# Optimization experiments

Measured on AMD Instinct MI355X. Metric: run time of the kernel, lower is better.

Reference implementation:

```python
import jax, jax.numpy as jnp
import numpy as np

N0, N1, N2 = 100000, 20000, 4000   # src(block0), dst(block0)=src(block1), dst(block1)
R = 3                               # number of relations
E0, E1 = 160000, 64000              # edges per relation per block
IN_FEATS, HID = 128, 128
TSS, RS = 64, 64
NTOT = 200000                       # global node count for tss/rs embed tables
F_IN = HID + TSS + RS               # IGConv input feature dim = 256


def _lin(key, fi, fo):
    k1, k2 = jax.random.split(key)
    s = float(1.0 / np.sqrt(fi))
    w = jax.random.uniform(k1, (fi, fo), minval=-s, maxval=s, dtype=jnp.float32)
    b = jax.random.uniform(k2, (fo,), minval=-s, maxval=s, dtype=jnp.float32)
    return w, b


def setup_inputs() -> dict:
    ks = jax.random.split(jax.random.key(0), 32)
    inp = {}
    inp["x_user"] = jax.random.normal(ks[0], (N0, IN_FEATS), dtype=jnp.float32)
    inp["tss_embed"] = jax.random.normal(ks[1], (NTOT, TSS), dtype=jnp.float32)
    inp["rs_embed"] = jax.random.normal(ks[2], (NTOT, RS), dtype=jnp.float32)
    inp["src_nid0"] = jax.random.randint(ks[3], (N0,), 0, NTOT)
    inp["src_nid1"] = jax.random.randint(ks[4], (N1,), 0, NTOT)
    inp["e0_src"] = jax.random.randint(ks[5], (R, E0), 0, N0)
    inp["e0_dst"] = jax.random.randint(ks[6], (R, E0), 0, N1)
    inp["e1_src"] = jax.random.randint(ks[7], (R, E1), 0, N1)
    inp["e1_dst"] = jax.random.randint(ks[8], (R, E1), 0, N2)
    inp["embed_w"], inp["embed_b"] = _lin(ks[9], IN_FEATS, HID)
    i = 10
    for l in (1, 2):
        for nm, fi in (("fc1", F_IN), ("fc2", 3 * F_IN), ("fc3", 2 * HID)):
            pw, pb = zip(*[_lin(jax.random.fold_in(ks[i], r), fi, HID) for r in range(R)])
            inp["l%d_%s_w" % (l, nm)] = jnp.stack(pw)  # [R, fi, HID]
            inp["l%d_%s_b" % (l, nm)] = jnp.stack(pb)  # [R, HID]
            i += 1
    inp["attn_w1"], inp["attn_b1"] = _lin(ks[i], HID, HID)
    inp["attn_w2"] = _lin(ks[i + 1], HID, 1)[0]  # Linear(hid,1,bias=False)
    inp["pred_w"], inp["pred_b"] = _lin(ks[i + 2], HID, 1)
    return inp


def _igconv(src_feat, dst_feat, esrc, edst, n_dst, fc1w, fc1b, fc2w, fc2b, fc3w, fc3b):
    # copy_u gather then max/mean/sum segment reductions over destination nodes
    m = src_feat[esrc]                                   # [E, F]
    s = jax.ops.segment_sum(m, edst, num_segments=n_dst)
    deg = jax.ops.segment_sum(jnp.ones(esrc.shape, m.dtype), edst, num_segments=n_dst)
    mean = s / jnp.maximum(deg, 1.0)[:, None]
    mx = jax.ops.segment_max(m, edst, num_segments=n_dst)
    mx = jnp.where(deg[:, None] > 0, mx, jnp.zeros_like(mx))  # DGL zeros for isolated dst
    msg = jnp.concatenate([mx, mean, s], axis=1)         # [n_dst, 3F]
    inp = jnp.concatenate([msg @ fc2w + fc2b, dst_feat @ fc1w + fc1b], axis=1)
    return jax.nn.relu(inp) @ fc3w + fc3b                # [n_dst, HID]


def _attn(z, w1, b1, w2):
    # SemanticAttention: z [N, R, HID]
    w = (jnp.tanh(z @ w1 + b1) @ w2).mean(0)             # [R, 1]
    beta = jax.nn.softmax(w, axis=0)                     # [R, 1]
    return (beta[None] * z).sum(1)                       # [N, HID]


def _forward(x_user, tss_embed, rs_embed, embed_w, embed_b,
             l1_fc1_w, l1_fc1_b, l1_fc2_w, l1_fc2_b, l1_fc3_w, l1_fc3_b,
             l2_fc1_w, l2_fc1_b, l2_fc2_w, l2_fc2_b, l2_fc3_w, l2_fc3_b,
             attn_w1, attn_b1, attn_w2, pred_w, pred_b,
             src_nid0, src_nid1, e0_src, e0_dst, e1_src, e1_dst):
    u0 = x_user @ embed_w + embed_b                      # self.embed
    feat0 = jnp.concatenate([u0, tss_embed[src_nid0], rs_embed[src_nid0]], axis=1)  # [N0,256]
    conv1 = jax.vmap(lambda es, ed, w1, b1, w2, b2, w3, b3:
                     _igconv(feat0, feat0[:N1], es, ed, N1, w1, b1, w2, b2, w3, b3))
    z1 = conv1(e0_src, e0_dst, l1_fc1_w, l1_fc1_b, l1_fc2_w, l1_fc2_b, l1_fc3_w, l1_fc3_b)  # [R,N1,HID]
    h1 = jax.nn.relu(_attn(jnp.transpose(z1, (1, 0, 2)), attn_w1, attn_b1, attn_w2))  # [N1,HID]
    feat1 = jnp.concatenate([h1, tss_embed[src_nid1], rs_embed[src_nid1]], axis=1)    # [N1,256]
    conv2 = jax.vmap(lambda es, ed, w1, b1, w2, b2, w3, b3:
                     _igconv(feat1, feat1[:N2], es, ed, N2, w1, b1, w2, b2, w3, b3))
    z2 = conv2(e1_src, e1_dst, l2_fc1_w, l2_fc1_b, l2_fc2_w, l2_fc2_b, l2_fc3_w, l2_fc3_b)  # [R,N2,HID]
    h2 = _attn(jnp.transpose(z2, (1, 0, 2)), attn_w1, attn_b1, attn_w2)              # [N2,HID]
    return jax.nn.sigmoid(h2 @ pred_w + pred_b)          # [N2,1]


def reference(x_user, tss_embed, rs_embed, src_nid0, src_nid1,
              e0_src, e0_dst, e1_src, e1_dst, embed_w, embed_b,
              l1_fc1_w, l1_fc1_b, l1_fc2_w, l1_fc2_b, l1_fc3_w, l1_fc3_b,
              l2_fc1_w, l2_fc1_b, l2_fc2_w, l2_fc2_b, l2_fc3_w, l2_fc3_b,
              attn_w1, attn_b1, attn_w2, pred_w, pred_b):
    return _forward(x_user, tss_embed, rs_embed, embed_w, embed_b,
                    l1_fc1_w, l1_fc1_b, l1_fc2_w, l1_fc2_b, l1_fc3_w, l1_fc3_b,
                    l2_fc1_w, l2_fc1_b, l2_fc2_w, l2_fc2_b, l2_fc3_w, l2_fc3_b,
                    attn_w1, attn_b1, attn_w2, pred_w, pred_b,
                    src_nid0, src_nid1, e0_src, e0_dst, e1_src, e1_dst)
```

## Files before the change

### kernel.cpp

```cpp
#include <hip/hip_runtime.h>
#include <math.h>


typedef short s16x8 __attribute__((ext_vector_type(8)));
typedef float f32x4 __attribute__((ext_vector_type(4)));

__device__ __forceinline__ ushort f2bf(float f) {
  unsigned u = __float_as_uint(f);
  return (ushort)((u + 0x7FFFu + ((u >> 16) & 1u)) >> 16);
}
__device__ __forceinline__ float bf2f(unsigned hbits) {
  return __uint_as_float(hbits << 16);
}
__device__ __forceinline__ unsigned pack2(float lo, float hi) {
  return (unsigned)f2bf(lo) | ((unsigned)f2bf(hi) << 16);
}

struct PrepAll {
  const float* src[8];
  ushort* dst[8];
  int K[8];
  int total[8];
};

__global__ __launch_bounds__(256) void prep_all(PrepAll P)
{
  int t = blockIdx.z;
  int off = blockIdx.x * 256 + threadIdx.x;
  if (off >= P.total[t]) return;
  int K = P.K[t];
  int k = off % K;
  int n = (off / K) & 127;
  int r = off / (K * 128);
  P.dst[t][off] = f2bf(P.src[t][((size_t)r * K + k) * 128 + n]);
}

struct GemmDesc {
  const void* A; int lda; size_t aStride; int aKind;
  const ushort* Wt; size_t wStride;
  const float* bias; int biasStride;
  void* C; int ldc; size_t cStride; int cKind;
  int M, K, relu;
  const ushort* aggM; const ushort* aggS; const float* invdeg;
  size_t aggStride; int invStride;
  const int* gnid; const float* gtss; const float* grs;
};

__global__ __launch_bounds__(256) void gemm_mfma(GemmDesc d0, GemmDesc d1)
{
  const GemmDesc d = blockIdx.z ? d1 : d0;
  const int r = blockIdx.y;
  __shared__ ushort As[128 * 32];
  __shared__ ushort Bs[128 * 32];

  const int tid = threadIdx.x;
  const int wave = tid >> 6, lane = tid & 63;
  const int m16 = lane & 15, quad = lane >> 4;
  const int rowBase = blockIdx.x * 128;
  const ushort* Wt = d.Wt + (size_t)r * d.wStride;

  f32x4 acc[2][8];
  #pragma unroll
  for (int i = 0; i < 2; ++i)
    #pragma unroll
    for (int j = 0; j < 8; ++j)
      #pragma unroll
      for (int p = 0; p < 4; ++p) acc[i][j][p] = 0.f;

  for (int k0 = 0; k0 < d.K; k0 += 32) {
    __syncthreads();
    if (d.aKind == 1) {
      const ushort* Ab = (const ushort*)d.A + (size_t)r * d.aStride;
      #pragma unroll
      for (int i = 0; i < 2; ++i) {
        int q = tid + 256 * i;
        int row = q >> 2, c = (q & 3) * 8;
        int grow = rowBase + row;
        uint4 v = make_uint4(0, 0, 0, 0);
        if (grow < d.M) v = *(const uint4*)(Ab + (size_t)grow * d.lda + k0 + c);
        *(uint4*)&As[row * 32 + c] = v;
      }
    } else if (d.aKind == 0) {
      const float* Ab = (const float*)d.A + (size_t)r * d.aStride;
      #pragma unroll
      for (int i = 0; i < 4; ++i) {
        int q = tid + 256 * i;
        int row = q >> 3, c = (q & 7) * 4;
        int grow = rowBase + row;
        float4 f = make_float4(0.f, 0.f, 0.f, 0.f);
        if (grow < d.M) f = *(const float4*)(Ab + (size_t)grow * d.lda + k0 + c);
        uint2 pk; pk.x = pack2(f.x, f.y); pk.y = pack2(f.z, f.w);
        *(uint2*)&As[row * 32 + c] = pk;
      }
    } else {
      int seg = k0 >> 8, jj = k0 & 255;
      const ushort* Ab = (seg == 0 ? d.aggM : d.aggS) + (size_t)r * d.aggStride;
      const float* idg = d.invdeg + (size_t)r * d.invStride;
      #pragma unroll
      for (int i = 0; i < 2; ++i) {
        int q = tid + 256 * i;
        int row = q >> 2, c = (q & 3) * 8;
        int grow = rowBase + row;
        uint4 v = make_uint4(0, 0, 0, 0);
        if (grow < d.M) {
          v = *(const uint4*)(Ab + (size_t)grow * 256 + jj + c);
          if (seg == 1) {
            float s = idg[grow];
            v.x = pack2(bf2f(v.x & 0xFFFFu) * s, bf2f(v.x >> 16) * s);
            v.y = pack2(bf2f(v.y & 0xFFFFu) * s, bf2f(v.y >> 16) * s);
            v.z = pack2(bf2f(v.z & 0xFFFFu) * s, bf2f(v.z >> 16) * s);
            v.w = pack2(bf2f(v.w & 0xFFFFu) * s, bf2f(v.w >> 16) * s);
          }
        }
        *(uint4*)&As[row * 32 + c] = v;
      }
    }
    #pragma unroll
    for (int i = 0; i < 2; ++i) {
      int q = tid + 256 * i;
      int col = q >> 2, c = (q & 3) * 8;
      uint4 v = *(const uint4*)(Wt + (size_t)col * d.K + k0 + c);
      *(uint4*)&Bs[col * 32 + c] = v;
    }
    __syncthreads();

    s16x8 af[2], bfr[8];
    af[0] = *(const s16x8*)&As[(wave * 32 + m16) * 32 + quad * 8];
    af[1] = *(const s16x8*)&As[(wave * 32 + 16 + m16) * 32 + quad * 8];
    #pragma unroll
    for (int j = 0; j < 8; ++j)
      bfr[j] = *(const s16x8*)&Bs[(j * 16 + m16) * 32 + quad * 8];
    #pragma unroll
    for (int i = 0; i < 2; ++i)
      #pragma unroll
      for (int j = 0; j < 8; ++j)
        acc[i][j] = __builtin_amdgcn_mfma_f32_16x16x32_bf16(af[i], bfr[j], acc[i][j], 0, 0, 0);
  }

  const float* bias = d.bias + (size_t)r * d.biasStride;
  float bcol[8];
  #pragma unroll
  for (int j = 0; j < 8; ++j) bcol[j] = bias[j * 16 + m16];

  #pragma unroll
  for (int i = 0; i < 2; ++i) {
    #pragma unroll
    for (int p = 0; p < 4; ++p) {
      int grow = rowBase + wave * 32 + i * 16 + quad * 4 + p;
      if (grow >= d.M) continue;
      if (d.cKind == 0) {
        float* Crow = (float*)d.C + (size_t)r * d.cStride + (size_t)grow * d.ldc;
        #pragma unroll
        for (int j = 0; j < 8; ++j) {
          float v = acc[i][j][p] + bcol[j];
          if (d.relu) v = fmaxf(v, 0.f);
          Crow[j * 16 + m16] = v;
        }
      } else {
        ushort* Crow = (ushort*)d.C + (size_t)r * d.cStride + (size_t)grow * d.ldc;
        #pragma unroll
        for (int j = 0; j < 8; ++j) {
          float v = acc[i][j][p] + bcol[j];
          if (d.relu) v = fmaxf(v, 0.f);
          Crow[j * 16 + m16] = f2bf(v);
        }
      }
    }
  }

  if (d.gnid) {
    #pragma unroll
    for (int i = 0; i < 16; ++i) {
      int q = tid + 256 * i;
      int row = q >> 5, c = q & 31;
      int grow = rowBase + row;
      if (grow >= d.M) continue;
      int id = d.gnid[grow];
      float4 v = (c < 16) ? *(const float4*)(d.gtss + (size_t)id * 64 + c * 4)
                          : *(const float4*)(d.grs  + (size_t)id * 64 + (c - 16) * 4);
      uint2 pk; pk.x = pack2(v.x, v.y); pk.y = pack2(v.z, v.w);
      *(uint2*)((ushort*)d.C + (size_t)grow * d.ldc + 128 + c * 4) = pk;
    }
  }
}

__global__ __launch_bounds__(256) void attn_mfma(
    const float* __restrict__ z, const ushort* __restrict__ w1t,
    const float* __restrict__ b1, const float* __restrict__ w2,
    int N, float* __restrict__ wsum)
{
  const int r = blockIdx.y;
  const float* zr = z + (size_t)r * N * 128;
  __shared__ ushort As[128 * 32];
  __shared__ ushort Bs[128 * 32];

  const int tid = threadIdx.x;
  const int wave = tid >> 6, lane = tid & 63;
  const int m16 = lane & 15, quad = lane >> 4;
  const int rowBase = blockIdx.x * 128;

  f32x4 acc[2][8];
  #pragma unroll
  for (int i = 0; i < 2; ++i)
    #pragma unroll
    for (int j = 0; j < 8; ++j)
      #pragma unroll
      for (int p = 0; p < 4; ++p) acc[i][j][p] = 0.f;

  for (int k0 = 0; k0 < 128; k0 += 32) {
    __syncthreads();
    #pragma unroll
    for (int i = 0; i < 4; ++i) {
      int q = tid + 256 * i;
      int row = q >> 3, c = (q & 7) * 4;
      int grow = rowBase + row;
      float4 f = make_float4(0.f, 0.f, 0.f, 0.f);
      if (grow < N) f = *(const float4*)(zr + (size_t)grow * 128 + k0 + c);
      uint2 pk; pk.x = pack2(f.x, f.y); pk.y = pack2(f.z, f.w);
      *(uint2*)&As[row * 32 + c] = pk;
    }
    #pragma unroll
    for (int i = 0; i < 2; ++i) {
      int q = tid + 256 * i;
      int col = q >> 2, c = (q & 3) * 8;
      uint4 v = *(const uint4*)(w1t + (size_t)col * 128 + k0 + c);
      *(uint4*)&Bs[col * 32 + c] = v;
    }
    __syncthreads();

    s16x8 af[2], bfr[8];
    af[0] = *(const s16x8*)&As[(wave * 32 + m16) * 32 + quad * 8];
    af[1] = *(const s16x8*)&As[(wave * 32 + 16 + m16) * 32 + quad * 8];
    #pragma unroll
    for (int j = 0; j < 8; ++j)
      bfr[j] = *(const s16x8*)&Bs[(j * 16 + m16) * 32 + quad * 8];
    #pragma unroll
    for (int i = 0; i < 2; ++i)
      #pragma unroll
      for (int j = 0; j < 8; ++j)
        acc[i][j] = __builtin_amdgcn_mfma_f32_16x16x32_bf16(af[i], bfr[j], acc[i][j], 0, 0, 0);
  }

  float b1c[8], w2c[8];
  #pragma unroll
  for (int j = 0; j < 8; ++j) { b1c[j] = b1[j * 16 + m16]; w2c[j] = w2[j * 16 + m16]; }

  float local = 0.f;
  #pragma unroll
  for (int i = 0; i < 2; ++i)
    #pragma unroll
    for (int p = 0; p < 4; ++p) {
      int grow = rowBase + wave * 32 + i * 16 + quad * 4 + p;
      if (grow >= N) continue;
      #pragma unroll
      for (int j = 0; j < 8; ++j)
        local += tanhf(acc[i][j][p] + b1c[j]) * w2c[j];
    }
  #pragma unroll
  for (int o = 32; o > 0; o >>= 1) local += __shfl_down(local, o);
  __shared__ float red[4];
  if (lane == 0) red[wave] = local;
  __syncthreads();
  if (tid == 0) atomicAdd(&wsum[r], red[0] + red[1] + red[2] + red[3]);
}

__global__ void count_deg(const int* __restrict__ edst, int E, int N, int* __restrict__ deg)
{
  int e = blockIdx.x * blockDim.x + threadIdx.x;
  int r = blockIdx.y;
  if (e < E) atomicAdd(&deg[r * N + edst[(size_t)r * E + e]], 1);
}

__global__ __launch_bounds__(1024) void scan_kernel(
    const int* __restrict__ deg, int* __restrict__ rowptr,
    int* __restrict__ cursor, int N)
{
  __shared__ int wtot[16];
  __shared__ int chunk_total_s;
  const int tid = threadIdx.x, lane = tid & 63, wid = tid >> 6;
  int running = 0;
  for (int base = 0; base < N; base += 4096) {
    int i0 = base + tid * 4;
    int d0 = 0, d1 = 0, d2 = 0, d3 = 0;
    if (i0 < N) {
      if (i0 + 3 < N) { int4 t = *(const int4*)(deg + i0); d0 = t.x; d1 = t.y; d2 = t.z; d3 = t.w; }
      else { d0 = deg[i0]; if (i0+1 < N) d1 = deg[i0+1]; if (i0+2 < N) d2 = deg[i0+2]; }
    }
    int tsum = d0 + d1 + d2 + d3;
    int incl = tsum;
    #pragma unroll
    for (int o = 1; o < 64; o <<= 1) {
      int t = __shfl_up(incl, o);
      if (lane >= o) incl += t;
    }
    if (lane == 63) wtot[wid] = incl;
    __syncthreads();
    if (wid == 0 && lane < 16) {
      int t = wtot[lane];
      int inc = t;
      #pragma unroll
      for (int o = 1; o < 16; o <<= 1) {
        int u = __shfl_up(inc, o);
        if (lane >= o) inc += u;
      }
      wtot[lane] = inc - t;
      if (lane == 15) chunk_total_s = inc;
    }
    __syncthreads();
    int excl = running + wtot[wid] + (incl - tsum);
    if (i0 < N) {
      int e1 = excl + d0, e2 = e1 + d1, e3 = e2 + d2;
      if (i0 + 3 < N) {
        *(int4*)(rowptr + i0) = make_int4(excl, e1, e2, e3);
        *(int4*)(cursor + i0) = make_int4(0, 0, 0, 0);
      } else {
        rowptr[i0] = excl; cursor[i0] = 0;
        if (i0+1 < N) { rowptr[i0+1] = e1; cursor[i0+1] = 0; }
        if (i0+2 < N) { rowptr[i0+2] = e2; cursor[i0+2] = 0; }
      }
    }
    running += chunk_total_s;
    __syncthreads();
  }
  if (tid == 0) rowptr[N] = running;
}

__global__ void fill_csr(const int* __restrict__ esrc, const int* __restrict__ edst,
                         int E, int N, const int* __restrict__ rowptr,
                         int* __restrict__ cursor, int* __restrict__ csr)
{
  int e = blockIdx.x * blockDim.x + threadIdx.x;
  int r = blockIdx.y;
  if (e >= E) return;
  int d = r * N + edst[(size_t)r * E + e];
  int pos = atomicAdd(&cursor[d], 1);
  csr[rowptr[d] + pos] = esrc[(size_t)r * E + e];
}

__global__ __launch_bounds__(256) void agg_kernel(
    const ushort* __restrict__ feat, const int* __restrict__ csr,
    const int* __restrict__ rowptr, int N, int c0, int cr, int CH,
    ushort* __restrict__ aggS, ushort* __restrict__ aggM, float* __restrict__ invdeg)
{
  const int wid = threadIdx.x >> 6, lane = threadIdx.x & 63;
  const int node = blockIdx.x * 4 + wid;
  if (node >= cr) return;
  const int g = blockIdx.y * N + c0 + node;
  const int o = blockIdx.y * CH + node;
  const int start = rowptr[g], end = rowptr[g + 1];
  const int j = lane * 4;
  float s0 = 0.f, s1 = 0.f, s2 = 0.f, s3 = 0.f;
  float m0 = -INFINITY, m1 = -INFINITY, m2 = -INFINITY, m3 = -INFINITY;
  int e = start;
  for (; e + 4 <= end; e += 4) {
    int sa = csr[e], sb = csr[e+1], sc = csr[e+2], sd = csr[e+3];
    uint2 va = *(const uint2*)(feat + (size_t)sa * 256 + j);
    uint2 vb = *(const uint2*)(feat + (size_t)sb * 256 + j);
    uint2 vc = *(const uint2*)(feat + (size_t)sc * 256 + j);
    uint2 vd = *(const uint2*)(feat + (size_t)sd * 256 + j);
    float a0, a1, a2, a3;
    a0 = bf2f(va.x & 0xFFFFu); a1 = bf2f(va.x >> 16); a2 = bf2f(va.y & 0xFFFFu); a3 = bf2f(va.y >> 16);
    s0 += a0; s1 += a1; s2 += a2; s3 += a3;
    m0 = fmaxf(m0, a0); m1 = fmaxf(m1, a1); m2 = fmaxf(m2, a2); m3 = fmaxf(m3, a3);
    a0 = bf2f(vb.x & 0xFFFFu); a1 = bf2f(vb.x >> 16); a2 = bf2f(vb.y & 0xFFFFu); a3 = bf2f(vb.y >> 16);
    s0 += a0; s1 += a1; s2 += a2; s3 += a3;
    m0 = fmaxf(m0, a0); m1 = fmaxf(m1, a1); m2 = fmaxf(m2, a2); m3 = fmaxf(m3, a3);
    a0 = bf2f(vc.x & 0xFFFFu); a1 = bf2f(vc.x >> 16); a2 = bf2f(vc.y & 0xFFFFu); a3 = bf2f(vc.y >> 16);
    s0 += a0; s1 += a1; s2 += a2; s3 += a3;
    m0 = fmaxf(m0, a0); m1 = fmaxf(m1, a1); m2 = fmaxf(m2, a2); m3 = fmaxf(m3, a3);
    a0 = bf2f(vd.x & 0xFFFFu); a1 = bf2f(vd.x >> 16); a2 = bf2f(vd.y & 0xFFFFu); a3 = bf2f(vd.y >> 16);
    s0 += a0; s1 += a1; s2 += a2; s3 += a3;
    m0 = fmaxf(m0, a0); m1 = fmaxf(m1, a1); m2 = fmaxf(m2, a2); m3 = fmaxf(m3, a3);
  }
  for (; e < end; ++e) {
    int src = csr[e];
    uint2 v = *(const uint2*)(feat + (size_t)src * 256 + j);
    float a0 = bf2f(v.x & 0xFFFFu), a1 = bf2f(v.x >> 16);
    float a2 = bf2f(v.y & 0xFFFFu), a3 = bf2f(v.y >> 16);
    s0 += a0; s1 += a1; s2 += a2; s3 += a3;
    m0 = fmaxf(m0, a0); m1 = fmaxf(m1, a1); m2 = fmaxf(m2, a2); m3 = fmaxf(m3, a3);
  }
  if (end == start) { m0 = m1 = m2 = m3 = 0.f; }
  uint2 ps; ps.x = pack2(s0, s1); ps.y = pack2(s2, s3);
  *(uint2*)(aggS + (size_t)o * 256 + j) = ps;
  uint2 pm; pm.x = pack2(m0, m1); pm.y = pack2(m2, m3);
  *(uint2*)(aggM + (size_t)o * 256 + j) = pm;
  if (lane == 0) invdeg[o] = 1.f / fmaxf((float)(end - start), 1.f);
}

__global__ void beta_kernel(const float* __restrict__ wsum, float invN, float* __restrict__ beta) {
  float w0 = wsum[0] * invN, w1 = wsum[1] * invN, w2 = wsum[2] * invN;
  float m  = fmaxf(w0, fmaxf(w1, w2));
  float e0 = expf(w0 - m), e1 = expf(w1 - m), e2 = expf(w2 - m);
  float s  = e0 + e1 + e2;
  beta[0] = e0 / s; beta[1] = e1 / s; beta[2] = e2 / s;
}

__global__ __launch_bounds__(256) void combine1_kernel(
    const float* __restrict__ z1, const float* __restrict__ beta,
    const float* __restrict__ tss, const float* __restrict__ rs,
    const int* __restrict__ nid, int N, ushort* __restrict__ feat1)
{
  int n = blockIdx.x, t = threadIdx.x;
  size_t NH = (size_t)N * 128;
  if (t < 128) {
    float v = beta[0] * z1[(size_t)n*128 + t] + beta[1] * z1[NH + (size_t)n*128 + t]
            + beta[2] * z1[2*NH + (size_t)n*128 + t];
    feat1[(size_t)n*256 + t] = f2bf(fmaxf(v, 0.f));
  } else {
    int j = t - 128;
    int id = nid[n];
    float v = (j < 64) ? tss[(size_t)id*64 + j] : rs[(size_t)id*64 + j - 64];
    feat1[(size_t)n*256 + t] = f2bf(v);
  }
}

__global__ __launch_bounds__(128) void combine2_pred(
    const float* __restrict__ z2, const float* __restrict__ beta, int N,
    const float* __restrict__ pw, const float* __restrict__ pb, float* __restrict__ out)
{
  int n = blockIdx.x, t = threadIdx.x;
  size_t NH = (size_t)N * 128;
  float h = beta[0] * z2[(size_t)n*128 + t] + beta[1] * z2[NH + (size_t)n*128 + t]
          + beta[2] * z2[2*NH + (size_t)n*128 + t];
  float p = h * pw[t];
  #pragma unroll
  for (int o = 32; o > 0; o >>= 1) p += __shfl_down(p, o);
  __shared__ float red[2];
  if ((t & 63) == 0) red[t >> 6] = p;
  __syncthreads();
  if (t == 0) {
    float v = red[0] + red[1] + pb[0];
    out[n] = 1.f / (1.f + expf(-v));
  }
}

extern "C" void kernel_launch(void* const* d_in, const int* in_sizes, int n_in,
                              void* d_out, int out_size, void* d_ws, size_t ws_size,
                              hipStream_t stream)
{
  const float* x_user  = (const float*)d_in[0];
  const float* tss     = (const float*)d_in[1];
  const float* rs      = (const float*)d_in[2];
  const int* src_nid0  = (const int*)d_in[3];
  const int* src_nid1  = (const int*)d_in[4];
  const int* e0_src    = (const int*)d_in[5];
  const int* e0_dst    = (const int*)d_in[6];
  const int* e1_src    = (const int*)d_in[7];
  const int* e1_dst    = (const int*)d_in[8];
  const float* embed_w = (const float*)d_in[9];
  const float* embed_b = (const float*)d_in[10];
  const float* l1w[3]  = {(const float*)d_in[11], (const float*)d_in[13], (const float*)d_in[15]};
  const float* l1b[3]  = {(const float*)d_in[12], (const float*)d_in[14], (const float*)d_in[16]};
  const float* l2w[3]  = {(const float*)d_in[17], (const float*)d_in[19], (const float*)d_in[21]};
  const float* l2b[3]  = {(const float*)d_in[18], (const float*)d_in[20], (const float*)d_in[22]};
  const float* attn_w1 = (const float*)d_in[23];
  const float* attn_b1 = (const float*)d_in[24];
  const float* attn_w2 = (const float*)d_in[25];
  const float* pred_w  = (const float*)d_in[26];
  const float* pred_b  = (const float*)d_in[27];
  float* out = (float*)d_out;

  const int N0 = in_sizes[0] / 128;
  const int N1 = in_sizes[4];
  const int N2 = out_size;
  const int E0 = in_sizes[5] / 3;
  const int E1 = in_sizes[7] / 3;

  char* wp = (char*)d_ws;
  auto walloc = [&](size_t bytes) {
    char* p = wp; wp += (bytes + 255) & ~(size_t)255; return p;
  };
  ushort* feat0  = (ushort*)walloc((size_t)N0 * 256 * 2);
  ushort* inp    = (ushort*)walloc((size_t)3 * N1 * 256 * 2);
  float*  z      = (float*)walloc((size_t)3 * N1 * 128 * 4);
  ushort* wt_emb = (ushort*)walloc((size_t)128 * 128 * 2);
  ushort* wt_attn = (ushort*)walloc((size_t)128 * 128 * 2);
  ushort* wt_fc1[2], *wt_fc2[2], *wt_fc3[2];
  for (int l = 0; l < 2; ++l) {
    wt_fc1[l] = (ushort*)walloc((size_t)3 * 256 * 128 * 2);
    wt_fc2[l] = (ushort*)walloc((size_t)3 * 768 * 128 * 2);
    wt_fc3[l] = (ushort*)walloc((size_t)3 * 256 * 128 * 2);
  }
  int*   degcnt = (int*)walloc((size_t)3 * N1 * 4);
  int*   rowptr = (int*)walloc((size_t)(3 * N1 + 1) * 4);
  int*   csr    = (int*)walloc((size_t)3 * E0 * 4);
  float* small  = (float*)walloc(256);
  float* wsum = small;
  float* beta = small + 4;
  ushort* feat1 = feat0;

  size_t used = (size_t)(wp - (char*)d_ws);
  size_t avail = (ws_size > used + 65536) ? (ws_size - used - 65536) : 0;
  const size_t per_row = (size_t)3 * (2 * 256 * 2 + 4 + 64);
  int CH = (int)(avail / per_row);
  if (CH > N1) CH = N1;
  if (CH < 1024) CH = 1024;
  ushort* aggS   = (ushort*)walloc((size_t)3 * CH * 256 * 2);
  ushort* aggM   = (ushort*)walloc((size_t)3 * CH * 256 * 2);
  float*  invdeg = (float*)walloc((size_t)3 * CH * 4);
  (void)n_in;

  {
    PrepAll P;
    P.src[0] = embed_w;  P.dst[0] = wt_emb;    P.K[0] = 128; P.total[0] = 128 * 128;
    P.src[1] = attn_w1;  P.dst[1] = wt_attn;   P.K[1] = 128; P.total[1] = 128 * 128;
    P.src[2] = l1w[0];   P.dst[2] = wt_fc1[0]; P.K[2] = 256; P.total[2] = 3 * 256 * 128;
    P.src[3] = l1w[1];   P.dst[3] = wt_fc2[0]; P.K[3] = 768; P.total[3] = 3 * 768 * 128;
    P.src[4] = l1w[2];   P.dst[4] = wt_fc3[0]; P.K[4] = 256; P.total[4] = 3 * 256 * 128;
    P.src[5] = l2w[0];   P.dst[5] = wt_fc1[1]; P.K[5] = 256; P.total[5] = 3 * 256 * 128;
    P.src[6] = l2w[1];   P.dst[6] = wt_fc2[1]; P.K[6] = 768; P.total[6] = 3 * 768 * 128;
    P.src[7] = l2w[2];   P.dst[7] = wt_fc3[1]; P.K[7] = 256; P.total[7] = 3 * 256 * 128;
    prep_all<<<dim3((3 * 768 * 128 + 255) / 256, 1, 8), 256, 0, stream>>>(P);
  }

  GemmDesc dz = {};

  {
    GemmDesc d{};
    d.A = x_user; d.lda = 128; d.aStride = 0; d.aKind = 0;
    d.Wt = wt_emb; d.wStride = 0; d.bias = embed_b; d.biasStride = 0;
    d.C = feat0; d.ldc = 256; d.cStride = 0; d.cKind = 1;
    d.M = N0; d.K = 128; d.relu = 0;
    d.aggM = aggM; d.aggS = aggS; d.invdeg = invdeg; d.aggStride = 0; d.invStride = 0;
    d.gnid = src_nid0; d.gtss = tss; d.grs = rs;
    gemm_mfma<<<dim3((N0 + 127) / 128, 1, 1), 256, 0, stream>>>(d, dz);
  }

  for (int layer = 0; layer < 2; ++layer) {
    const ushort* featS = layer ? feat1 : feat0;
    int Nd = layer ? N2 : N1;
    int E  = layer ? E1 : E0;
    const int* es = layer ? e1_src : e0_src;
    const int* ed = layer ? e1_dst : e0_dst;
    const float* const* lb = layer ? l2b : l1b;

    hipMemsetAsync(degcnt, 0, (size_t)3 * Nd * 4, stream);
    count_deg<<<dim3((E + 255) / 256, 3), 256, 0, stream>>>(ed, E, Nd, degcnt);
    scan_kernel<<<1, 1024, 0, stream>>>(degcnt, rowptr, degcnt, 3 * Nd);
    fill_csr<<<dim3((E + 255) / 256, 3), 256, 0, stream>>>(es, ed, E, Nd, rowptr, degcnt, csr);

    for (int c0 = 0; c0 < Nd; c0 += CH) {
      int cr = (Nd - c0 < CH) ? (Nd - c0) : CH;
      agg_kernel<<<dim3((cr + 3) / 4, 3), 256, 0, stream>>>(
          featS, csr, rowptr, Nd, c0, cr, CH, aggS, aggM, invdeg);
      GemmDesc d2{};
      d2.A = nullptr; d2.lda = 0; d2.aStride = 0; d2.aKind = 2;
      d2.Wt = wt_fc2[layer]; d2.wStride = (size_t)768 * 128; d2.bias = lb[1]; d2.biasStride = 128;
      d2.C = inp + (size_t)c0 * 256; d2.ldc = 256; d2.cStride = (size_t)Nd * 256; d2.cKind = 1;
      d2.M = cr; d2.K = 768; d2.relu = 1;
      d2.aggM = aggM; d2.aggS = aggS; d2.invdeg = invdeg;
      d2.aggStride = (size_t)CH * 256; d2.invStride = CH;
      GemmDesc d1{};
      d1.A = featS + (size_t)c0 * 256; d1.lda = 256; d1.aStride = 0; d1.aKind = 1;
      d1.Wt = wt_fc1[layer]; d1.wStride = (size_t)256 * 128; d1.bias = lb[0]; d1.biasStride = 128;
      d1.C = inp + 128 + (size_t)c0 * 256; d1.ldc = 256; d1.cStride = (size_t)Nd * 256; d1.cKind = 1;
      d1.M = cr; d1.K = 256; d1.relu = 1;
      d1.aggM = aggM; d1.aggS = aggS; d1.invdeg = invdeg; d1.aggStride = 0; d1.invStride = 0;
      gemm_mfma<<<dim3((cr + 127) / 128, 3, 2), 256, 0, stream>>>(d2, d1);
    }
    {
      GemmDesc d3{};
      d3.A = inp; d3.lda = 256; d3.aStride = (size_t)N1 * 0 + (size_t)Nd * 256; d3.aKind = 1;
      d3.Wt = wt_fc3[layer]; d3.wStride = (size_t)256 * 128; d3.bias = lb[2]; d3.biasStride = 128;
      d3.C = z; d3.ldc = 128; d3.cStride = (size_t)Nd * 128; d3.cKind = 0;
      d3.M = Nd; d3.K = 256; d3.relu = 0;
      d3.aggM = aggM; d3.aggS = aggS; d3.invdeg = invdeg; d3.aggStride = 0; d3.invStride = 0;
      gemm_mfma<<<dim3((Nd + 127) / 128, 3, 1), 256, 0, stream>>>(d3, dz);
    }

    hipMemsetAsync(wsum, 0, 3 * sizeof(float), stream);
    attn_mfma<<<dim3((Nd + 127) / 128, 3), 256, 0, stream>>>(z, wt_attn, attn_b1, attn_w2, Nd, wsum);
    beta_kernel<<<1, 1, 0, stream>>>(wsum, 1.0f / (float)Nd, beta);

    if (layer == 0) {
      combine1_kernel<<<N1, 256, 0, stream>>>(z, beta, tss, rs, src_nid1, N1, feat1);
    } else {
      combine2_pred<<<N2, 128, 0, stream>>>(z, beta, N2, pred_w, pred_b, out);
    }
  }
}
```

Baseline: 570.0 us.

## Load A fragments directly from global, stage 128-wide K chunks of W in LDS

The GEMM and attention kernels now use 64-row tiles. Each wave loads its A fragment straight from global memory into registers, so there is no A staging in shared memory. Weights are staged 128 K at a time in a fragment-ordered LDS layout, which cuts barriers from one per 32-K step to one per 128-K chunk and doubles the grid size. The cost is that A global loads are no longer cooperative or coalesced across the block, and each weight tile is reloaded by twice as many blocks.

```diff
diff --git a/kernel.cpp b/kernel.cpp
--- a/kernel.cpp
+++ b/kernel.cpp
@@ -50,136 +50,113 @@
 {
   const GemmDesc d = blockIdx.z ? d1 : d0;
   const int r = blockIdx.y;
-  __shared__ ushort As[128 * 32];
-  __shared__ ushort Bs[128 * 32];
+  __shared__ __align__(16) ushort Bs[2048 * 8];
 
   const int tid = threadIdx.x;
   const int wave = tid >> 6, lane = tid & 63;
   const int m16 = lane & 15, quad = lane >> 4;
-  const int rowBase = blockIdx.x * 128;
+  const int rowBase = blockIdx.x * 64;
+  const int row = rowBase + wave * 16 + m16;
+  const bool rowOK = row < d.M;
   const ushort* Wt = d.Wt + (size_t)r * d.wStride;
 
-  f32x4 acc[2][8];
-  #pragma unroll
-  for (int i = 0; i < 2; ++i)
-    #pragma unroll
-    for (int j = 0; j < 8; ++j)
+  f32x4 acc[8];
+  #pragma unroll
+  for (int j = 0; j < 8; ++j)
+    #pragma unroll
+    for (int p = 0; p < 4; ++p) acc[j][p] = 0.f;
+
+  float idg = 1.f;
+  if (d.aKind == 2 && rowOK) idg = d.invdeg[(size_t)r * d.invStride + row];
+
+  const ushort* Ab16 = (const ushort*)d.A + (size_t)r * d.aStride;
+  const float*  Ab32 = (const float*)d.A + (size_t)r * d.aStride;
+
+  for (int c0 = 0; c0 < d.K; c0 += 128) {
+    if (c0) __syncthreads();
+    #pragma unroll
+    for (int i = 0; i < 8; ++i) {
+      int q = tid + 256 * i;
+      int col = ((q >> 6) & 7) * 16 + (q & 15);
+      int kk  = c0 + (q >> 9) * 32 + ((q >> 4) & 3) * 8;
+      *(uint4*)&Bs[q * 8] = *(const uint4*)(Wt + (size_t)col * d.K + kk);
+    }
+    __syncthreads();
+
+    #pragma unroll
+    for (int ks = 0; ks < 4; ++ks) {
+      const int k0 = c0 + ks * 32;
+      uint4 pk = make_uint4(0u, 0u, 0u, 0u);
+      if (rowOK) {
+        if (d.aKind == 1) {
+          pk = *(const uint4*)(Ab16 + (size_t)row * d.lda + k0 + quad * 8);
+        } else if (d.aKind == 0) {
+          float4 fa = *(const float4*)(Ab32 + (size_t)row * d.lda + k0 + quad * 8);
+          float4 fb = *(const float4*)(Ab32 + (size_t)row * d.lda + k0 + quad * 8 + 4);
+          pk.x = pack2(fa.x, fa.y); pk.y = pack2(fa.z, fa.w);
+          pk.z = pack2(fb.x, fb.y); pk.w = pack2(fb.z, fb.w);
+        } else {
+          int seg = k0 >> 8;
+          int jj  = (k0 & 255) + quad * 8;
+          const ushort* Ag = (seg == 0 ? d.aggM : d.aggS) + (size_t)r * d.aggStride;
+          pk = *(const uint4*)(Ag + (size_t)row * 256 + jj);
+          if (seg == 1) {
+            pk.x = pack2(bf2f(pk.x & 0xFFFFu) * idg, bf2f(pk.x >> 16) * idg);
+            pk.y = pack2(bf2f(pk.y & 0xFFFFu) * idg, bf2f(pk.y >> 16) * idg);
+            pk.z = pack2(bf2f(pk.z & 0xFFFFu) * idg, bf2f(pk.z >> 16) * idg);
+            pk.w = pack2(bf2f(pk.w & 0xFFFFu) * idg, bf2f(pk.w >> 16) * idg);
+          }
+        }
+      }
+      s16x8 af = *(s16x8*)&pk;
       #pragma unroll
-      for (int p = 0; p < 4; ++p) acc[i][j][p] = 0.f;
-
-  for (int k0 = 0; k0 < d.K; k0 += 32) {
-    __syncthreads();
-    if (d.aKind == 1) {
-      const ushort* Ab = (const ushort*)d.A + (size_t)r * d.aStride;
+      for (int j = 0; j < 8; ++j) {
+        s16x8 bf = *(const s16x8*)&Bs[((ks * 8 + j) * 64 + lane) * 8];
+        acc[j] = __builtin_amdgcn_mfma_f32_16x16x32_bf16(af, bf, acc[j], 0, 0, 0);
+      }
+    }
+  }
+
+  const float* bias = d.bias + (size_t)r * d.biasStride;
+  float bcol[8];
+  #pragma unroll
+  for (int j = 0; j < 8; ++j) bcol[j] = bias[j * 16 + m16];
+
+  #pragma unroll
+  for (int p = 0; p < 4; ++p) {
+    int grow = rowBase + wave * 16 + quad * 4 + p;
+    if (grow >= d.M) continue;
+    if (d.cKind == 0) {
+      float* Crow = (float*)d.C + (size_t)r * d.cStride + (size_t)grow * d.ldc;
       #pragma unroll
-      for (int i = 0; i < 2; ++i) {
-        int q = tid + 256 * i;
-        int row = q >> 2, c = (q & 3) * 8;
-        int grow = rowBase + row;
-        uint4 v = make_uint4(0, 0, 0, 0);
-        if (grow < d.M) v = *(const uint4*)(Ab + (size_t)grow * d.lda + k0 + c);
-        *(uint4*)&As[row * 32 + c] = v;
-      }
-    } else if (d.aKind == 0) {
-      const float* Ab = (const float*)d.A + (size_t)r * d.aStride;
-      #pragma unroll
-      for (int i = 0; i < 4; ++i) {
-        int q = tid + 256 * i;
-        int row = q >> 3, c = (q & 7) * 4;
-        int grow = rowBase + row;
-        float4 f = make_float4(0.f, 0.f, 0.f, 0.f);
-        if (grow < d.M) f = *(const float4*)(Ab + (size_t)grow * d.lda + k0 + c);
-        uint2 pk; pk.x = pack2(f.x, f.y); pk.y = pack2(f.z, f.w);
-        *(uint2*)&As[row * 32 + c] = pk;
+      for (int j = 0; j < 8; ++j) {
+        float v = acc[j][p] + bcol[j];
+        if (d.relu) v = fmaxf(v, 0.f);
+        Crow[j * 16 + m16] = v;
       }
     } else {
-      int seg = k0 >> 8, jj = k0 & 255;
-      const ushort* Ab = (seg == 0 ? d.aggM : d.aggS) + (size_t)r * d.aggStride;
-      const float* idg = d.invdeg + (size_t)r * d.invStride;
+      ushort* Crow = (ushort*)d.C + (size_t)r * d.cStride + (size_t)grow * d.ldc;
       #pragma unroll
-      for (int i = 0; i < 2; ++i) {
-        int q = tid + 256 * i;
-        int row = q >> 2, c = (q & 3) * 8;
-        int grow = rowBase + row;
-        uint4 v = make_uint4(0, 0, 0, 0);
-        if (grow < d.M) {
-          v = *(const uint4*)(Ab + (size_t)grow * 256 + jj + c);
-          if (seg == 1) {
-            float s = idg[grow];
-            v.x = pack2(bf2f(v.x & 0xFFFFu) * s, bf2f(v.x >> 16) * s);
-            v.y = pack2(bf2f(v.y & 0xFFFFu) * s, bf2f(v.y >> 16) * s);
-            v.z = pack2(bf2f(v.z & 0xFFFFu) * s, bf2f(v.z >> 16) * s);
-            v.w = pack2(bf2f(v.w & 0xFFFFu) * s, bf2f(v.w >> 16) * s);
-          }
-        }
-        *(uint4*)&As[row * 32 + c] = v;
+      for (int j = 0; j < 8; ++j) {
+        float v = acc[j][p] + bcol[j];
+        if (d.relu) v = fmaxf(v, 0.f);
+        Crow[j * 16 + m16] = f2bf(v);
       }
     }
-    #pragma unroll
-    for (int i = 0; i < 2; ++i) {
+  }
+
+  if (d.gnid) {
+    #pragma unroll
+    for (int i = 0; i < 8; ++i) {
       int q = tid + 256 * i;
-      int col = q >> 2, c = (q & 3) * 8;
-      uint4 v = *(const uint4*)(Wt + (size_t)col * d.K + k0 + c);
-      *(uint4*)&Bs[col * 32 + c] = v;
-    }
-    __syncthreads();
-
-    s16x8 af[2], bfr[8];
-    af[0] = *(const s16x8*)&As[(wave * 32 + m16) * 32 + quad * 8];
-    af[1] = *(const s16x8*)&As[(wave * 32 + 16 + m16) * 32 + quad * 8];
-    #pragma unroll
-    for (int j = 0; j < 8; ++j)
-      bfr[j] = *(const s16x8*)&Bs[(j * 16 + m16) * 32 + quad * 8];
-    #pragma unroll
-    for (int i = 0; i < 2; ++i)
-      #pragma unroll
-      for (int j = 0; j < 8; ++j)
-        acc[i][j] = __builtin_amdgcn_mfma_f32_16x16x32_bf16(af[i], bfr[j], acc[i][j], 0, 0, 0);
-  }
-
-  const float* bias = d.bias + (size_t)r * d.biasStride;
-  float bcol[8];
-  #pragma unroll
-  for (int j = 0; j < 8; ++j) bcol[j] = bias[j * 16 + m16];
-
-  #pragma unroll
-  for (int i = 0; i < 2; ++i) {
-    #pragma unroll
-    for (int p = 0; p < 4; ++p) {
-      int grow = rowBase + wave * 32 + i * 16 + quad * 4 + p;
-      if (grow >= d.M) continue;
-      if (d.cKind == 0) {
-        float* Crow = (float*)d.C + (size_t)r * d.cStride + (size_t)grow * d.ldc;
-        #pragma unroll
-        for (int j = 0; j < 8; ++j) {
-          float v = acc[i][j][p] + bcol[j];
-          if (d.relu) v = fmaxf(v, 0.f);
-          Crow[j * 16 + m16] = v;
-        }
-      } else {
-        ushort* Crow = (ushort*)d.C + (size_t)r * d.cStride + (size_t)grow * d.ldc;
-        #pragma unroll
-        for (int j = 0; j < 8; ++j) {
-          float v = acc[i][j][p] + bcol[j];
-          if (d.relu) v = fmaxf(v, 0.f);
-          Crow[j * 16 + m16] = f2bf(v);
-        }
-      }
-    }
-  }
-
-  if (d.gnid) {
-    #pragma unroll
-    for (int i = 0; i < 16; ++i) {
-      int q = tid + 256 * i;
-      int row = q >> 5, c = q & 31;
-      int grow = rowBase + row;
+      int grow = rowBase + (q >> 5);
+      int c = q & 31;
       if (grow >= d.M) continue;
       int id = d.gnid[grow];
       float4 v = (c < 16) ? *(const float4*)(d.gtss + (size_t)id * 64 + c * 4)
                           : *(const float4*)(d.grs  + (size_t)id * 64 + (c - 16) * 4);
-      uint2 pk; pk.x = pack2(v.x, v.y); pk.y = pack2(v.z, v.w);
-      *(uint2*)((ushort*)d.C + (size_t)grow * d.ldc + 128 + c * 4) = pk;
+      uint2 g; g.x = pack2(v.x, v.y); g.y = pack2(v.z, v.w);
+      *(uint2*)((ushort*)d.C + (size_t)grow * d.ldc + 128 + c * 4) = g;
     }
   }
 }
@@ -191,71 +168,61 @@
 {
   const int r = blockIdx.y;
   const float* zr = z + (size_t)r * N * 128;
-  __shared__ ushort As[128 * 32];
-  __shared__ ushort Bs[128 * 32];
+  __shared__ __align__(16) ushort Bs[2048 * 8];
 
   const int tid = threadIdx.x;
   const int wave = tid >> 6, lane = tid & 63;
   const int m16 = lane & 15, quad = lane >> 4;
-  const int rowBase = blockIdx.x * 128;
-
-  f32x4 acc[2][8];
-  #pragma unroll
-  for (int i = 0; i < 2; ++i)
+  const int rowBase = blockIdx.x * 64;
+  const int row = rowBase + wave * 16 + m16;
+  const bool rowOK = row < N;
+
+  f32x4 acc[8];
+  #pragma unroll
+  for (int j = 0; j < 8; ++j)
+    #pragma unroll
+    for (int p = 0; p < 4; ++p) acc[j][p] = 0.f;
+
+  #pragma unroll
+  for (int i = 0; i < 8; ++i) {
+    int q = tid + 256 * i;
+    int col = ((q >> 6) & 7) * 16 + (q & 15);
+    int kk  = (q >> 9) * 32 + ((q >> 4) & 3) * 8;
+    *(uint4*)&Bs[q * 8] = *(const uint4*)(w1t + (size_t)col * 128 + kk);
+  }
+  __syncthreads();
+
+  #pragma unroll
+  for (int ks = 0; ks < 4; ++ks) {
+    const int k0 = ks * 32;
+    uint4 pk = make_uint4(0u, 0u, 0u, 0u);
+    if (rowOK) {
+      float4 fa = *(const float4*)(zr + (size_t)row * 128 + k0 + quad * 8);
+      float4 fb = *(const float4*)(zr + (size_t)row * 128 + k0 + quad * 8 + 4);
+      pk.x = pack2(fa.x, fa.y); pk.y = pack2(fa.z, fa.w);
+      pk.z = pack2(fb.x, fb.y); pk.w = pack2(fb.z, fb.w);
+    }
+    s16x8 af = *(s16x8*)&pk;
+    #pragma unroll
+    for (int j = 0; j < 8; ++j) {
+      s16x8 bf = *(const s16x8*)&Bs[((ks * 8 + j) * 64 + lane) * 8];
+      acc[j] = __builtin_amdgcn_mfma_f32_16x16x32_bf16(af, bf, acc[j], 0, 0, 0);
+    }
+  }
+
+  float b1c[8], w2c[8];
+  #pragma unroll
+  for (int j = 0; j < 8; ++j) { b1c[j] = b1[j * 16 + m16]; w2c[j] = w2[j * 16 + m16]; }
+
+  float local = 0.f;
+  #pragma unroll
+  for (int p = 0; p < 4; ++p) {
+    int grow = rowBase + wave * 16 + quad * 4 + p;
+    if (grow >= N) continue;
     #pragma unroll
     for (int j = 0; j < 8; ++j)
-      #pragma unroll
-      for (int p = 0; p < 4; ++p) acc[i][j][p] = 0.f;
-
-  for (int k0 = 0; k0 < 128; k0 += 32) {
-    __syncthreads();
-    #pragma unroll
-    for (int i = 0; i < 4; ++i) {
-      int q = tid + 256 * i;
-      int row = q >> 3, c = (q & 7) * 4;
-      int grow = rowBase + row;
-      float4 f = make_float4(0.f, 0.f, 0.f, 0.f);
-      if (grow < N) f = *(const float4*)(zr + (size_t)grow * 128 + k0 + c);
-      uint2 pk; pk.x = pack2(f.x, f.y); pk.y = pack2(f.z, f.w);
-      *(uint2*)&As[row * 32 + c] = pk;
-    }
-    #pragma unroll
-    for (int i = 0; i < 2; ++i) {
-      int q = tid + 256 * i;
-      int col = q >> 2, c = (q & 3) * 8;
-      uint4 v = *(const uint4*)(w1t + (size_t)col * 128 + k0 + c);
-      *(uint4*)&Bs[col * 32 + c] = v;
-    }
-    __syncthreads();
-
-    s16x8 af[2], bfr[8];
-    af[0] = *(const s16x8*)&As[(wave * 32 + m16) * 32 + quad * 8];
-    af[1] = *(const s16x8*)&As[(wave * 32 + 16 + m16) * 32 + quad * 8];
-    #pragma unroll
-    for (int j = 0; j < 8; ++j)
-      bfr[j] = *(const s16x8*)&Bs[(j * 16 + m16) * 32 + quad * 8];
-    #pragma unroll
-    for (int i = 0; i < 2; ++i)
-      #pragma unroll
-      for (int j = 0; j < 8; ++j)
-        acc[i][j] = __builtin_amdgcn_mfma_f32_16x16x32_bf16(af[i], bfr[j], acc[i][j], 0, 0, 0);
-  }
-
-  float b1c[8], w2c[8];
-  #pragma unroll
-  for (int j = 0; j < 8; ++j) { b1c[j] = b1[j * 16 + m16]; w2c[j] = w2[j * 16 + m16]; }
-
-  float local = 0.f;
-  #pragma unroll
-  for (int i = 0; i < 2; ++i)
-    #pragma unroll
-    for (int p = 0; p < 4; ++p) {
-      int grow = rowBase + wave * 32 + i * 16 + quad * 4 + p;
-      if (grow >= N) continue;
-      #pragma unroll
-      for (int j = 0; j < 8; ++j)
-        local += tanhf(acc[i][j][p] + b1c[j]) * w2c[j];
-    }
+      local += tanhf(acc[j][p] + b1c[j]) * w2c[j];
+  }
   #pragma unroll
   for (int o = 32; o > 0; o >>= 1) local += __shfl_down(local, o);
   __shared__ float red[4];
@@ -524,7 +491,7 @@
     d.M = N0; d.K = 128; d.relu = 0;
     d.aggM = aggM; d.aggS = aggS; d.invdeg = invdeg; d.aggStride = 0; d.invStride = 0;
     d.gnid = src_nid0; d.gtss = tss; d.grs = rs;
-    gemm_mfma<<<dim3((N0 + 127) / 128, 1, 1), 256, 0, stream>>>(d, dz);
+    gemm_mfma<<<dim3((N0 + 63) / 64, 1, 1), 256, 0, stream>>>(d, dz);
   }
 
   for (int layer = 0; layer < 2; ++layer) {
@@ -557,7 +524,7 @@
       d1.C = inp + 128 + (size_t)c0 * 256; d1.ldc = 256; d1.cStride = (size_t)Nd * 256; d1.cKind = 1;
       d1.M = cr; d1.K = 256; d1.relu = 1;
       d1.aggM = aggM; d1.aggS = aggS; d1.invdeg = invdeg; d1.aggStride = 0; d1.invStride = 0;
-      gemm_mfma<<<dim3((cr + 127) / 128, 3, 2), 256, 0, stream>>>(d2, d1);
+      gemm_mfma<<<dim3((cr + 63) / 64, 3, 2), 256, 0, stream>>>(d2, d1);
     }
     {
       GemmDesc d3{};
@@ -566,11 +533,11 @@
       d3.C = z; d3.ldc = 128; d3.cStride = (size_t)Nd * 128; d3.cKind = 0;
       d3.M = Nd; d3.K = 256; d3.relu = 0;
       d3.aggM = aggM; d3.aggS = aggS; d3.invdeg = invdeg; d3.aggStride = 0; d3.invStride = 0;
-      gemm_mfma<<<dim3((Nd + 127) / 128, 3, 1), 256, 0, stream>>>(d3, dz);
+      gemm_mfma<<<dim3((Nd + 63) / 64, 3, 1), 256, 0, stream>>>(d3, dz);
     }
 
     hipMemsetAsync(wsum, 0, 3 * sizeof(float), stream);
-    attn_mfma<<<dim3((Nd + 127) / 128, 3), 256, 0, stream>>>(z, wt_attn, attn_b1, attn_w2, Nd, wsum);
+    attn_mfma<<<dim3((Nd + 63) / 64, 3), 256, 0, stream>>>(z, wt_attn, attn_b1, attn_w2, Nd, wsum);
     beta_kernel<<<1, 1, 0, stream>>>(wsum, 1.0f / (float)Nd, beta);
 
     if (layer == 0) {
```

Result: faster. 546.8 us (-4.1%).
